# Kernel optimization log

Hardware: AMD Instinct MI355X
Metric: run time of the kernel (lower is better)

The kernel has to match this reference:

```python
import jax, jax.numpy as jnp
import numpy as np
from functools import partial

N = 10000      # nodes
E = 100000     # edges
WIDTH = 64     # node hidden width
KER_W = 1024   # kernel MLP hidden width
KER_IN = 6     # edge feature dim
DEPTH = 6


def setup_inputs() -> dict:
    key = jax.random.key(0)
    ks = jax.random.split(key, 16)

    def glorot(k, shape):
        fan_in = shape[0]
        return jax.random.normal(k, shape, dtype=jnp.float32) / np.sqrt(fan_in)

    inp = {
        "x": jax.random.normal(ks[0], (N, 1), dtype=jnp.float32),
        "edge_index": jax.random.randint(ks[1], (2, E), 0, N, dtype=jnp.int32),
        "edge_attr": jax.random.uniform(ks[2], (E, KER_IN), dtype=jnp.float32),
        # fc1: in_width=1 -> width
        "fc1_w": glorot(ks[3], (1, WIDTH)),
        "fc1_b": jnp.zeros((WIDTH,), jnp.float32),
        # kernel DenseNet: ker_in -> ker_width -> ker_width -> width**2 (ReLU between)
        "k1_w": glorot(ks[4], (KER_IN, KER_W)),
        "k1_b": jnp.zeros((KER_W,), jnp.float32),
        "k2_w": glorot(ks[5], (KER_W, KER_W)),
        "k2_b": jnp.zeros((KER_W,), jnp.float32),
        "k3_w": glorot(ks[6], (KER_W, WIDTH * WIDTH)),
        "k3_b": jnp.zeros((WIDTH * WIDTH,), jnp.float32),
        # NNConv_old root weight + bias
        "root_w": glorot(ks[7], (WIDTH, WIDTH)),
        "conv_b": jnp.zeros((WIDTH,), jnp.float32),
        # fc2: width -> 1
        "fc2_w": glorot(ks[8], (WIDTH, 1)),
        "fc2_b": jnp.zeros((1,), jnp.float32),
    }
    return inp


def reference(x, edge_index, edge_attr, fc1_w, fc1_b, k1_w, k1_b, k2_w, k2_b,
              k3_w, k3_b, root_w, conv_b, fc2_w, fc2_b):
    src = edge_index[0]  # x_j (source, gathered)
    dst = edge_index[1]  # aggregation target

    # Per-edge kernel MLP -> [E, width, width]. edge_attr is constant across
    # depth iterations, so compute the edge weights once (same math).
    h = jax.nn.relu(edge_attr @ k1_w + k1_b)
    h = jax.nn.relu(h @ k2_w + k2_b)
    ew = (h @ k3_w + k3_b).reshape(E, WIDTH, WIDTH)

    # mean aggregation denominators (scatter_mean semantics: deg clamped to 1)
    deg = jax.ops.segment_sum(jnp.ones((E,), jnp.float32), dst, num_segments=N)
    deg = jnp.maximum(deg, 1.0)[:, None]  # [N,1]

    z = x @ fc1_w + fc1_b  # [N, width]
    for _ in range(DEPTH):
        msg = jnp.einsum('ei,eio->eo', z[src], ew)            # gather + per-edge matmul
        agg = jax.ops.segment_sum(msg, dst, num_segments=N)   # scatter-add
        agg = agg / deg                                       # mean
        z = jax.nn.relu(agg + z @ root_w + conv_b)
    return z @ fc2_w + fc2_b  # [N, 1]
```

## Files before the change

### kernel.cpp

```cpp
#include <hip/hip_runtime.h>
#include <hip/hip_bf16.h>

#define N_NODES 10000
#define N_EDGES 100000
#define DEPTH   6
#define E_CHUNK 12500

typedef __attribute__((ext_vector_type(8))) short short8;
typedef __attribute__((ext_vector_type(4))) float f32x4;
typedef unsigned short u16;

__device__ __forceinline__ float bf2f(u16 u) {
    union { float f; unsigned int i; } v; v.i = ((unsigned int)u) << 16; return v.f;
}
__device__ __forceinline__ u16 f2bf(float f) {
    union { float f; unsigned int i; } v; v.f = f;
    unsigned int x = v.i;
    unsigned int r = (x + 0x7fffu + ((x >> 16) & 1u)) >> 16;
    return (u16)r;
}

__device__ __forceinline__ void gload_lds16(const void* g, void* s) {
    __builtin_amdgcn_global_load_lds((const __attribute__((address_space(1))) void*)g,
                                     (__attribute__((address_space(3))) void*)s, 16, 0, 0);
}

__global__ void k2_transpose_kernel(const float* __restrict__ k2w, u16* __restrict__ k2T) {
    int idx = blockIdx.x * 256 + threadIdx.x;
    int n = idx >> 10, k = idx & 1023;
    k2T[idx] = f2bf(k2w[k * 1024 + n]);
}
__global__ void k3_permT_kernel(const float* __restrict__ k3w, u16* __restrict__ k3pT) {
    int idx = blockIdx.x * 256 + threadIdx.x;
    int n = idx >> 10, c = idx & 1023;
    k3pT[idx] = f2bf(k3w[(size_t)c * 4096 + (n & 63) * 64 + (n >> 6)]);
}
__global__ void b3_permute_kernel(const float* __restrict__ b3, float* __restrict__ b3p) {
    int n = blockIdx.x * 256 + threadIdx.x;
    if (n >= 4096) return;
    b3p[n] = b3[(n & 63) * 64 + (n >> 6)];
}

__global__ void deg_kernel(const int* __restrict__ ei, float* __restrict__ deg) {
    int e = blockIdx.x * 256 + threadIdx.x;
    if (e < N_EDGES) atomicAdd(&deg[ei[N_EDGES + e]], 1.0f);
}

__global__ void gemm1_kernel(const float* __restrict__ ea, const float* __restrict__ k1w,
                             const float* __restrict__ k1b, u16* __restrict__ h1, int e0) {
    int idx = blockIdx.x * 256 + threadIdx.x;
    int c = idx & 1023;
    int e = (idx >> 10) + e0;
    float acc = k1b[c];
#pragma unroll
    for (int i = 0; i < 6; i++) acc += ea[e * 6 + i] * k1w[i * 1024 + c];
    h1[idx] = f2bf(fmaxf(acc, 0.0f));
}

template <int NOUT, bool RELU, bool FUSE_MSG>
__global__ __launch_bounds__(256) void gemm128_kernel(
    const u16* __restrict__ A, const u16* __restrict__ BT,
    const float* __restrict__ bias, u16* __restrict__ C, int M,
    const int* __restrict__ ei, const float* __restrict__ z,
    float* __restrict__ agg) {
    constexpr int K = 1024;
    __shared__ __align__(16) u16 Alds[128 * 32];
    __shared__ __align__(16) u16 Blds[128 * 32];

    const int t = threadIdx.x;
    const int lane = t & 63, w = t >> 6;
    const int wm = w >> 1, wn = w & 1;
    const int fm = lane & 15, q = lane >> 4;
    const int m0 = blockIdx.y * 128;
    const int n0 = blockIdx.x * 128;

    f32x4 acc[4][4];
#pragma unroll
    for (int a = 0; a < 4; a++)
#pragma unroll
        for (int b = 0; b < 4; b++) acc[a][b] = (f32x4){0.f, 0.f, 0.f, 0.f};

    int ar0 = m0 + (t >> 2);        if (ar0 >= M) ar0 = M - 1;
    int ar1 = m0 + 64 + (t >> 2);   if (ar1 >= M) ar1 = M - 1;
    const u16* gA0 = A + (size_t)ar0 * K + (t & 3) * 8;
    const u16* gA1 = A + (size_t)ar1 * K + (t & 3) * 8;
    const u16* gB0 = BT + (size_t)(n0 + (t >> 2)) * K + (t & 3) * 8;
    const u16* gB1 = BT + (size_t)(n0 + 64 + (t >> 2)) * K + (t & 3) * 8;
    u16* lA0 = &Alds[t * 8];
    u16* lA1 = &Alds[2048 + t * 8];
    u16* lB0 = &Blds[t * 8];
    u16* lB1 = &Blds[2048 + t * 8];

    for (int k0 = 0; k0 < K; k0 += 32) {
        gload_lds16(gA0 + k0, lA0);
        gload_lds16(gA1 + k0, lA1);
        gload_lds16(gB0 + k0, lB0);
        gload_lds16(gB1 + k0, lB1);
        __syncthreads();

        short8 af[4], bf[4];
#pragma unroll
        for (int mi = 0; mi < 4; mi++)
            af[mi] = *reinterpret_cast<const short8*>(&Alds[(wm * 64 + mi * 16 + fm) * 32 + q * 8]);
#pragma unroll
        for (int ni = 0; ni < 4; ni++)
            bf[ni] = *reinterpret_cast<const short8*>(&Blds[(wn * 64 + ni * 16 + fm) * 32 + q * 8]);
#pragma unroll
        for (int mi = 0; mi < 4; mi++)
#pragma unroll
            for (int ni = 0; ni < 4; ni++)
                acc[mi][ni] = __builtin_amdgcn_mfma_f32_16x16x32_bf16(af[mi], bf[ni], acc[mi][ni], 0, 0, 0);
        __syncthreads();
    }

    if (!FUSE_MSG) {
#pragma unroll
        for (int mi = 0; mi < 4; mi++) {
#pragma unroll
            for (int ni = 0; ni < 4; ni++) {
                int col = n0 + wn * 64 + ni * 16 + fm;
                float bsv = bias[col];
#pragma unroll
                for (int r = 0; r < 4; r++) {
                    int row = m0 + wm * 64 + mi * 16 + q * 4 + r;
                    if (row < M) {
                        float v = acc[mi][ni][r] + bsv;
                        if (RELU) v = fmaxf(v, 0.0f);
                        C[(size_t)row * NOUT + col] = f2bf(v);
                    }
                }
            }
        }
    } else {
        const int o = (n0 >> 6) + wn;
        float bsv[4];
        int iidx[4];
#pragma unroll
        for (int ni = 0; ni < 4; ni++) {
            bsv[ni] = bias[n0 + wn * 64 + ni * 16 + fm];
            iidx[ni] = ni * 16 + fm;
        }
#pragma unroll
        for (int mi = 0; mi < 4; mi++) {
#pragma unroll
            for (int r = 0; r < 4; r++) {
                int e = m0 + wm * 64 + mi * 16 + q * 4 + r;
                float partial = 0.f;
                int dst = 0;
                if (e < M) {
                    int src = ei[e];
                    dst = ei[N_EDGES + e];
                    const float* zs = z + (size_t)src * 64;
#pragma unroll
                    for (int ni = 0; ni < 4; ni++)
                        partial += (acc[mi][ni][r] + bsv[ni]) * zs[iidx[ni]];
                }
                partial += __shfl_xor(partial, 1);
                partial += __shfl_xor(partial, 2);
                partial += __shfl_xor(partial, 4);
                partial += __shfl_xor(partial, 8);
                if (fm == 0 && e < M) atomicAdd(&agg[(size_t)dst * 64 + o], partial);
            }
        }
    }
}

__global__ void z0_kernel(const float* __restrict__ x, const float* __restrict__ w,
                          const float* __restrict__ b, float* __restrict__ z) {
    int idx = blockIdx.x * 256 + threadIdx.x;
    int n = idx >> 6, o = idx & 63;
    z[idx] = x[n] * w[o] + b[o];
}

__global__ __launch_bounds__(256) void update_kernel(const float* __restrict__ zin,
                                                     const float* __restrict__ agg,
                                                     const float* __restrict__ deg,
                                                     const float* __restrict__ rootw,
                                                     const float* __restrict__ convb,
                                                     float* __restrict__ zout) {
    int n = blockIdx.x * 4 + (threadIdx.x >> 6);
    int o = threadIdx.x & 63;
    float r = convb[o];
    const float* zr = zin + (size_t)n * 64;
#pragma unroll 8
    for (int i = 0; i < 64; i++) r += zr[i] * rootw[i * 64 + o];
    float d = deg[n];
    d = d < 1.0f ? 1.0f : d;
    float v = agg[(size_t)n * 64 + o] / d + r;
    zout[(size_t)n * 64 + o] = fmaxf(v, 0.0f);
}

__global__ void final_kernel(const float* __restrict__ z, const float* __restrict__ w,
                             const float* __restrict__ b, float* __restrict__ out) {
    int n = blockIdx.x * 256 + threadIdx.x;
    if (n >= N_NODES) return;
    float acc = b[0];
#pragma unroll 8
    for (int o = 0; o < 64; o++) acc += z[(size_t)n * 64 + o] * w[o];
    out[n] = acc;
}

__global__ void dbg_kernel(float* __restrict__ out, float val, int n) {
    int i = blockIdx.x * 256 + threadIdx.x;
    if (i < n) out[i] = val;
}

extern "C" void kernel_launch(void* const* d_in, const int* in_sizes, int n_in,
                              void* d_out, int out_size, void* d_ws, size_t ws_size,
                              hipStream_t stream) {
    const float* x     = (const float*)d_in[0];
    const int*   ei    = (const int*)  d_in[1];
    const float* ea    = (const float*)d_in[2];
    const float* fc1w  = (const float*)d_in[3];
    const float* fc1b  = (const float*)d_in[4];
    const float* k1w   = (const float*)d_in[5];
    const float* k1b   = (const float*)d_in[6];
    const float* k2w   = (const float*)d_in[7];
    const float* k2b   = (const float*)d_in[8];
    const float* k3w   = (const float*)d_in[9];
    const float* k3b   = (const float*)d_in[10];
    const float* rootw = (const float*)d_in[11];
    const float* convb = (const float*)d_in[12];
    const float* fc2w  = (const float*)d_in[13];
    const float* fc2b  = (const float*)d_in[14];
    float* out = (float*)d_out;

    const size_t NEED = 249000000;
    if (ws_size < NEED) {
        dbg_kernel<<<(N_NODES + 255) / 256, 256, 0, stream>>>(out, (float)(ws_size >> 20), N_NODES);
        return;
    }

    char* p = (char*)d_ws;
    auto alloc = [&](size_t bytes) {
        char* r = p;
        p += (bytes + 255) & ~(size_t)255;
        return r;
    };
    u16*   h2   = (u16*)  alloc((size_t)N_EDGES * 1024 * 2);
    u16*   h1ch = (u16*)  alloc((size_t)E_CHUNK * 1024 * 2);
    u16*   k2T  = (u16*)  alloc((size_t)1024 * 1024 * 2);
    u16*   k3pT = (u16*)  alloc((size_t)4096 * 1024 * 2);
    float* b3p  = (float*)alloc(4096 * 4);
    float* zA   = (float*)alloc((size_t)N_NODES * 64 * 4);
    float* zB   = (float*)alloc((size_t)N_NODES * 64 * 4);
    float* agg  = (float*)alloc((size_t)N_NODES * 64 * 4);
    float* deg  = (float*)alloc((size_t)N_NODES * 4);

    hipMemsetAsync(deg, 0, (size_t)N_NODES * 4, stream);

    k2_transpose_kernel<<<(1024 * 1024) / 256, 256, 0, stream>>>(k2w, k2T);
    k3_permT_kernel<<<(4096 * 1024) / 256, 256, 0, stream>>>(k3w, k3pT);
    b3_permute_kernel<<<16, 256, 0, stream>>>(k3b, b3p);
    deg_kernel<<<(N_EDGES + 255) / 256, 256, 0, stream>>>(ei, deg);

    for (int e0 = 0; e0 < N_EDGES; e0 += E_CHUNK) {
        gemm1_kernel<<<(E_CHUNK * 1024) / 256, 256, 0, stream>>>(ea, k1w, k1b, h1ch, e0);
        dim3 g2(1024 / 128, (E_CHUNK + 127) / 128);
        gemm128_kernel<1024, true, false><<<g2, 256, 0, stream>>>(
            h1ch, k2T, k2b, h2 + (size_t)e0 * 1024, E_CHUNK, nullptr, nullptr, nullptr);
    }

    z0_kernel<<<(N_NODES * 64) / 256, 256, 0, stream>>>(x, fc1w, fc1b, zA);

    float* zin = zA;
    float* zout = zB;
    for (int d = 0; d < DEPTH; d++) {
        hipMemsetAsync(agg, 0, (size_t)N_NODES * 64 * 4, stream);
        dim3 g3(4096 / 128, (N_EDGES + 127) / 128);
        gemm128_kernel<4096, false, true><<<g3, 256, 0, stream>>>(
            h2, k3pT, b3p, nullptr, N_EDGES, ei, zin, agg);
        update_kernel<<<N_NODES / 4, 256, 0, stream>>>(zin, agg, deg, rootw, convb, zout);
        float* tmp = zin; zin = zout; zout = tmp;
    }

    final_kernel<<<(N_NODES + 255) / 256, 256, 0, stream>>>(zin, fc2w, fc2b, out);
}
```

Before: 7.544 ms.

## Restructure message GEMM to accumulate per-output partials and split out bias term

Result: slower. 14.11 ms (+87.0%).

```diff
diff --git a/kernel.cpp b/kernel.cpp
--- a/kernel.cpp
+++ b/kernel.cpp
@@ -30,15 +30,10 @@
     int n = idx >> 10, k = idx & 1023;
     k2T[idx] = f2bf(k2w[k * 1024 + n]);
 }
-__global__ void k3_permT_kernel(const float* __restrict__ k3w, u16* __restrict__ k3pT) {
+__global__ void k3_transpose_kernel(const float* __restrict__ k3w, u16* __restrict__ k3T) {
     int idx = blockIdx.x * 256 + threadIdx.x;
-    int n = idx >> 10, c = idx & 1023;
-    k3pT[idx] = f2bf(k3w[(size_t)c * 4096 + (n & 63) * 64 + (n >> 6)]);
-}
-__global__ void b3_permute_kernel(const float* __restrict__ b3, float* __restrict__ b3p) {
-    int n = blockIdx.x * 256 + threadIdx.x;
-    if (n >= 4096) return;
-    b3p[n] = b3[(n & 63) * 64 + (n >> 6)];
+    int col = idx >> 10, c = idx & 1023;
+    k3T[idx] = f2bf(k3w[(size_t)c * 4096 + col]);
 }
 
 __global__ void deg_kernel(const int* __restrict__ ei, float* __restrict__ deg) {
@@ -57,12 +52,11 @@
     h1[idx] = f2bf(fmaxf(acc, 0.0f));
 }
 
-template <int NOUT, bool RELU, bool FUSE_MSG>
-__global__ __launch_bounds__(256) void gemm128_kernel(
-    const u16* __restrict__ A, const u16* __restrict__ BT,
-    const float* __restrict__ bias, u16* __restrict__ C, int M,
-    const int* __restrict__ ei, const float* __restrict__ z,
-    float* __restrict__ agg) {
+template <int NOUT, bool RELU>
+__global__ __launch_bounds__(256) void gemm128_kernel(const u16* __restrict__ A,
+                                                      const u16* __restrict__ BT,
+                                                      const float* __restrict__ bias,
+                                                      u16* __restrict__ C, int M) {
     constexpr int K = 1024;
     __shared__ __align__(16) u16 Alds[128 * 32];
     __shared__ __align__(16) u16 Blds[128 * 32];
@@ -97,7 +91,6 @@
         gload_lds16(gB0 + k0, lB0);
         gload_lds16(gB1 + k0, lB1);
         __syncthreads();
-
         short8 af[4], bf[4];
 #pragma unroll
         for (int mi = 0; mi < 4; mi++)
@@ -113,53 +106,137 @@
         __syncthreads();
     }
 
-    if (!FUSE_MSG) {
+#pragma unroll
+    for (int mi = 0; mi < 4; mi++) {
+#pragma unroll
+        for (int ni = 0; ni < 4; ni++) {
+            int col = n0 + wn * 64 + ni * 16 + fm;
+            float bsv = bias[col];
+#pragma unroll
+            for (int r = 0; r < 4; r++) {
+                int row = m0 + wm * 64 + mi * 16 + q * 4 + r;
+                if (row < M) {
+                    float v = acc[mi][ni][r] + bsv;
+                    if (RELU) v = fmaxf(v, 0.0f);
+                    C[(size_t)row * NOUT + col] = f2bf(v);
+                }
+            }
+        }
+    }
+}
+
+__global__ __launch_bounds__(256) void gemm_msg_kernel(
+    const u16* __restrict__ A, const u16* __restrict__ BT,
+    const int* __restrict__ ei, const float* __restrict__ z,
+    float* __restrict__ agg, int M) {
+    constexpr int K = 1024;
+    __shared__ __align__(16) u16 Alds[128 * 32];
+    __shared__ __align__(16) u16 Blds[128 * 32];
+    __shared__ float zlds[128 * 64];
+
+    const int t = threadIdx.x;
+    const int lane = t & 63, w = t >> 6;
+    const int wm = w >> 1, wn = w & 1;
+    const int fm = lane & 15, q = lane >> 4;
+    const int m0 = blockIdx.y * 128;
+    const int g = blockIdx.x;
+
+    {
+        int row = t >> 1, half = t & 1;
+        int e = m0 + row; if (e >= M) e = M - 1;
+        int src = ei[e];
+        const float4* zr = (const float4*)(z + (size_t)src * 64 + half * 32);
+        float4* zd = (float4*)(&zlds[row * 64 + half * 32]);
+#pragma unroll
+        for (int j = 0; j < 8; j++) zd[j] = zr[j];
+    }
+
+    int ar0 = m0 + (t >> 2);        if (ar0 >= M) ar0 = M - 1;
+    int ar1 = m0 + 64 + (t >> 2);   if (ar1 >= M) ar1 = M - 1;
+    const u16* gA0 = A + (size_t)ar0 * K + (t & 3) * 8;
+    const u16* gA1 = A + (size_t)ar1 * K + (t & 3) * 8;
+    u16* lA0 = &Alds[t * 8];
+    u16* lA1 = &Alds[2048 + t * 8];
+    u16* lB0 = &Blds[t * 8];
+    u16* lB1 = &Blds[2048 + t * 8];
+
+    f32x4 msgreg[4][4];
+#pragma unroll
+    for (int a = 0; a < 4; a++)
+#pragma unroll
+        for (int b = 0; b < 4; b++) msgreg[a][b] = (f32x4){0.f, 0.f, 0.f, 0.f};
+
+    for (int nt = 0; nt < 8; nt++) {
+        const int n0 = g * 1024 + nt * 128;
+        const u16* gB0 = BT + (size_t)(n0 + (t >> 2)) * K + (t & 3) * 8;
+        const u16* gB1 = BT + (size_t)(n0 + 64 + (t >> 2)) * K + (t & 3) * 8;
+
+        f32x4 acc[4][4];
+#pragma unroll
+        for (int a = 0; a < 4; a++)
+#pragma unroll
+            for (int b = 0; b < 4; b++) acc[a][b] = (f32x4){0.f, 0.f, 0.f, 0.f};
+
+        for (int k0 = 0; k0 < K; k0 += 32) {
+            gload_lds16(gA0 + k0, lA0);
+            gload_lds16(gA1 + k0, lA1);
+            gload_lds16(gB0 + k0, lB0);
+            gload_lds16(gB1 + k0, lB1);
+            __syncthreads();
+            short8 af[4], bf[4];
+#pragma unroll
+            for (int mi = 0; mi < 4; mi++)
+                af[mi] = *reinterpret_cast<const short8*>(&Alds[(wm * 64 + mi * 16 + fm) * 32 + q * 8]);
+#pragma unroll
+            for (int ni = 0; ni < 4; ni++)
+                bf[ni] = *reinterpret_cast<const short8*>(&Blds[(wn * 64 + ni * 16 + fm) * 32 + q * 8]);
+#pragma unroll
+            for (int mi = 0; mi < 4; mi++)
+#pragma unroll
+                for (int ni = 0; ni < 4; ni++)
+                    acc[mi][ni] = __builtin_amdgcn_mfma_f32_16x16x32_bf16(af[mi], bf[ni], acc[mi][ni], 0, 0, 0);
+            __syncthreads();
+        }
+
+        const int i_idx = g * 16 + nt * 2 + wn;
 #pragma unroll
         for (int mi = 0; mi < 4; mi++) {
 #pragma unroll
-            for (int ni = 0; ni < 4; ni++) {
-                int col = n0 + wn * 64 + ni * 16 + fm;
-                float bsv = bias[col];
-#pragma unroll
-                for (int r = 0; r < 4; r++) {
-                    int row = m0 + wm * 64 + mi * 16 + q * 4 + r;
-                    if (row < M) {
-                        float v = acc[mi][ni][r] + bsv;
-                        if (RELU) v = fmaxf(v, 0.0f);
-                        C[(size_t)row * NOUT + col] = f2bf(v);
+            for (int r = 0; r < 4; r++) {
+                int el = wm * 64 + mi * 16 + q * 4 + r;
+                float zv = zlds[el * 64 + i_idx];
+#pragma unroll
+                for (int ni = 0; ni < 4; ni++)
+                    msgreg[mi][ni][r] += acc[mi][ni][r] * zv;
+            }
+        }
+    }
+
+    float* red = (float*)Alds;
+#pragma unroll
+    for (int mi = 0; mi < 4; mi++) {
+        __syncthreads();
+        if (wn == 1) {
+#pragma unroll
+            for (int r = 0; r < 4; r++)
+#pragma unroll
+                for (int ni = 0; ni < 4; ni++)
+                    red[(wm * 16 + q * 4 + r) * 64 + ni * 16 + fm] = msgreg[mi][ni][r];
+        }
+        __syncthreads();
+        if (wn == 0) {
+#pragma unroll
+            for (int r = 0; r < 4; r++) {
+                int e = m0 + wm * 64 + mi * 16 + q * 4 + r;
+                if (e < M) {
+                    int dst = ei[N_EDGES + e];
+#pragma unroll
+                    for (int ni = 0; ni < 4; ni++) {
+                        int o = ni * 16 + fm;
+                        float v = msgreg[mi][ni][r] + red[(wm * 16 + q * 4 + r) * 64 + o];
+                        atomicAdd(&agg[(size_t)dst * 64 + o], v);
                     }
                 }
-            }
-        }
-    } else {
-        const int o = (n0 >> 6) + wn;
-        float bsv[4];
-        int iidx[4];
-#pragma unroll
-        for (int ni = 0; ni < 4; ni++) {
-            bsv[ni] = bias[n0 + wn * 64 + ni * 16 + fm];
-            iidx[ni] = ni * 16 + fm;
-        }
-#pragma unroll
-        for (int mi = 0; mi < 4; mi++) {
-#pragma unroll
-            for (int r = 0; r < 4; r++) {
-                int e = m0 + wm * 64 + mi * 16 + q * 4 + r;
-                float partial = 0.f;
-                int dst = 0;
-                if (e < M) {
-                    int src = ei[e];
-                    dst = ei[N_EDGES + e];
-                    const float* zs = z + (size_t)src * 64;
-#pragma unroll
-                    for (int ni = 0; ni < 4; ni++)
-                        partial += (acc[mi][ni][r] + bsv[ni]) * zs[iidx[ni]];
-                }
-                partial += __shfl_xor(partial, 1);
-                partial += __shfl_xor(partial, 2);
-                partial += __shfl_xor(partial, 4);
-                partial += __shfl_xor(partial, 8);
-                if (fm == 0 && e < M) atomicAdd(&agg[(size_t)dst * 64 + o], partial);
             }
         }
     }
@@ -170,6 +247,27 @@
     int idx = blockIdx.x * 256 + threadIdx.x;
     int n = idx >> 6, o = idx & 63;
     z[idx] = x[n] * w[o] + b[o];
+}
+
+__global__ __launch_bounds__(256) void bz_kernel(const float* __restrict__ z,
+                                                 const float* __restrict__ b3,
+                                                 float* __restrict__ Bz) {
+    int n = blockIdx.x * 4 + (threadIdx.x >> 6);
+    int o = threadIdx.x & 63;
+    const float* zr = z + (size_t)n * 64;
+    float acc = 0.f;
+#pragma unroll 8
+    for (int i = 0; i < 64; i++) acc += zr[i] * b3[i * 64 + o];
+    Bz[(size_t)n * 64 + o] = acc;
+}
+
+__global__ __launch_bounds__(256) void bz_scatter_kernel(const int* __restrict__ ei,
+                                                         const float* __restrict__ Bz,
+                                                         float* __restrict__ agg) {
+    int e = blockIdx.x * 4 + (threadIdx.x >> 6);
+    int o = threadIdx.x & 63;
+    int src = ei[e], dst = ei[N_EDGES + e];
+    atomicAdd(&agg[(size_t)dst * 64 + o], Bz[(size_t)src * 64 + o]);
 }
 
 __global__ __launch_bounds__(256) void update_kernel(const float* __restrict__ zin,
@@ -225,7 +323,7 @@
     const float* fc2b  = (const float*)d_in[14];
     float* out = (float*)d_out;
 
-    const size_t NEED = 249000000;
+    const size_t NEED = 252000000;
     if (ws_size < NEED) {
         dbg_kernel<<<(N_NODES + 255) / 256, 256, 0, stream>>>(out, (float)(ws_size >> 20), N_NODES);
         return;
@@ -240,8 +338,8 @@
     u16*   h2   = (u16*)  alloc((size_t)N_EDGES * 1024 * 2);
     u16*   h1ch = (u16*)  alloc((size_t)E_CHUNK * 1024 * 2);
     u16*   k2T  = (u16*)  alloc((size_t)1024 * 1024 * 2);
-    u16*   k3pT = (u16*)  alloc((size_t)4096 * 1024 * 2);
-    float* b3p  = (float*)alloc(4096 * 4);
+    u16*   k3T  = (u16*)  alloc((size_t)4096 * 1024 * 2);
+    float* Bz   = (float*)alloc((size_t)N_NODES * 64 * 4);
     float* zA   = (float*)alloc((size_t)N_NODES * 64 * 4);
     float* zB   = (float*)alloc((size_t)N_NODES * 64 * 4);
     float* agg  = (float*)alloc((size_t)N_NODES * 64 * 4);
@@ -250,15 +348,14 @@
     hipMemsetAsync(deg, 0, (size_t)N_NODES * 4, stream);
 
     k2_transpose_kernel<<<(1024 * 1024) / 256, 256, 0, stream>>>(k2w, k2T);
-    k3_permT_kernel<<<(4096 * 1024) / 256, 256, 0, stream>>>(k3w, k3pT);
-    b3_permute_kernel<<<16, 256, 0, stream>>>(k3b, b3p);
+    k3_transpose_kernel<<<(4096 * 1024) / 256, 256, 0, stream>>>(k3w, k3T);
     deg_kernel<<<(N_EDGES + 255) / 256, 256, 0, stream>>>(ei, deg);
 
     for (int e0 = 0; e0 < N_EDGES; e0 += E_CHUNK) {
         gemm1_kernel<<<(E_CHUNK * 1024) / 256, 256, 0, stream>>>(ea, k1w, k1b, h1ch, e0);
         dim3 g2(1024 / 128, (E_CHUNK + 127) / 128);
-        gemm128_kernel<1024, true, false><<<g2, 256, 0, stream>>>(
-            h1ch, k2T, k2b, h2 + (size_t)e0 * 1024, E_CHUNK, nullptr, nullptr, nullptr);
+        gemm128_kernel<1024, true><<<g2, 256, 0, stream>>>(
+            h1ch, k2T, k2b, h2 + (size_t)e0 * 1024, E_CHUNK);
     }
 
     z0_kernel<<<(N_NODES * 64) / 256, 256, 0, stream>>>(x, fc1w, fc1b, zA);
@@ -267,9 +364,10 @@
     float* zout = zB;
     for (int d = 0; d < DEPTH; d++) {
         hipMemsetAsync(agg, 0, (size_t)N_NODES * 64 * 4, stream);
-        dim3 g3(4096 / 128, (N_EDGES + 127) / 128);
-        gemm128_kernel<4096, false, true><<<g3, 256, 0, stream>>>(
-            h2, k3pT, b3p, nullptr, N_EDGES, ei, zin, agg);
+        bz_kernel<<<N_NODES / 4, 256, 0, stream>>>(zin, k3b, Bz);
+        bz_scatter_kernel<<<N_EDGES / 4, 256, 0, stream>>>(ei, Bz, agg);
+        dim3 g3(4, (N_EDGES + 127) / 128);
+        gemm_msg_kernel<<<g3, 256, 0, stream>>>(h2, k3T, ei, zin, agg, N_EDGES);
         update_kernel<<<N_NODES / 4, 256, 0, stream>>>(zin, agg, deg, rootw, convb, zout);
         float* tmp = zin; zin = zout; zout = tmp;
     }
```
